# Kernel tuning notes

Measured on AMD Instinct MI355X. Metric: run time of the kernel, lower is better.

The kernel has to match this reference:

```python
import jax, jax.numpy as jnp
import numpy as np


def setup_inputs() -> dict:
    key = jax.random.key(0)
    k1, k2, k3, k4 = jax.random.split(key, 4)
    B, Lq, La, H = 8, 2048, 2048, 1024
    return {
        "q": jax.random.normal(k1, (B, Lq, H), dtype=jnp.float32),
        "a": jax.random.normal(k2, (B, La, H), dtype=jnp.float32),
        "w": jax.random.normal(k3, (H, H), dtype=jnp.float32),
        "b": jax.random.normal(k4, (H,), dtype=jnp.float32),
    }


def reference(q, a, w, b):
    # G = (q @ w + b) @ a^T : [B, Lq, La]
    G = jnp.einsum("bqh,hk->bqk", q, w) + b  # [B, Lq, H]
    G = jnp.einsum("bqh,bah->bqa", G, a)     # [B, Lq, La]
    # softmax over dim=1 (the q-length axis), no scaling
    G = jax.nn.softmax(G, axis=1)
    # H = G^T @ q : [B, La, H]
    return jnp.einsum("bqa,bqh->bah", G, q)
```

## Files before the change

kernel.cpp:

```cpp
#include <hip/hip_runtime.h>
#include <hip/hip_bf16.h>
#include <stdint.h>


typedef __bf16 bf16x8 __attribute__((ext_vector_type(8)));
typedef float f32x4 __attribute__((ext_vector_type(4)));
typedef unsigned int u32x4 __attribute__((ext_vector_type(4)));

typedef const __attribute__((address_space(1))) void* gas_t;
typedef __attribute__((address_space(3))) void* las_t;

__device__ __forceinline__ void gload_lds16(const void* g, void* l) {
    __builtin_amdgcn_global_load_lds((gas_t)g, (las_t)l, 16, 0, 0);
}

__device__ __forceinline__ unsigned cvt_pk_bf16(float a, float b) {
    unsigned r;
    asm("v_cvt_pk_bf16_f32 %0, %1, %2" : "=v"(r) : "v"(a), "v"(b));
    return r;
}

__device__ __forceinline__ void split8(f32x4 x0, f32x4 x1, bf16x8& hv, bf16x8& lv) {
    float xs[8];
#pragma unroll
    for (int i = 0; i < 4; ++i) { xs[i] = x0[i]; xs[4 + i] = x1[i]; }
    u32x4 hp, lp;
#pragma unroll
    for (int i = 0; i < 4; ++i) {
        float a = xs[2 * i], b = xs[2 * i + 1];
        unsigned p = cvt_pk_bf16(a, b);
        float ra = __uint_as_float(p << 16);
        float rb = __uint_as_float(p & 0xffff0000u);
        hp[i] = p;
        lp[i] = cvt_pk_bf16(a - ra, b - rb);
    }
    hv = __builtin_bit_cast(bf16x8, hp);
    lv = __builtin_bit_cast(bf16x8, lp);
}

#define MFMA16(a, b, c) __builtin_amdgcn_mfma_f32_16x16x32_bf16(a, b, c, 0, 0, 0)

template<bool BIAS, bool OUTSPLIT>
__global__ __launch_bounds__(256, 2) void gemm_splitAB(
    const float* __restrict__ A, const unsigned short* __restrict__ Bh,
    const unsigned short* __restrict__ Bl, const float* __restrict__ bias,
    float* __restrict__ C, unsigned short* __restrict__ Ph, unsigned short* __restrict__ Pl,
    int lda, int ldb, int ldc, int K, size_t sA, size_t sB, size_t sC)
{
    __shared__ char sm[32768];
    const int tid = threadIdx.x;
    const int lane = tid & 63, wid = tid >> 6;
    const int wr = wid >> 1, wc = wid & 1;
    const int bm = blockIdx.y * 128, bn = blockIdx.x * 128;

    const float* Ag = A + (size_t)blockIdx.z * sA;
    const unsigned short* Bhg = Bh + (size_t)blockIdx.z * sB;
    const unsigned short* Blg = Bl + (size_t)blockIdx.z * sB;

    const int a_rl = lane >> 3, a_s = lane & 7;
    const int a_kslot = a_s ^ a_rl;
    const int b_rl = lane >> 2, b_s = lane & 3;
    const int b_kslot = b_s ^ (b_rl & 3);

    const int frow = lane & 15, fkg = lane >> 4;

    f32x4 acc[4][4] = {};

    for (int k0 = 0; k0 < K; k0 += 32) {
        __syncthreads();
#pragma unroll
        for (int j = 0; j < 4; ++j) {
            int i = wid * 4 + j;
            int row = i * 8 + a_rl;
            gload_lds16(Ag + (size_t)(bm + row) * lda + (k0 + a_kslot * 4),
                        sm + i * 1024);
        }
#pragma unroll
        for (int j = 0; j < 2; ++j) {
            int i = wid * 2 + j;
            int row = i * 16 + b_rl;
            size_t goff = (size_t)(bn + row) * ldb + (k0 + b_kslot * 8);
            gload_lds16(Bhg + goff, sm + 16384 + i * 1024);
            gload_lds16(Blg + goff, sm + 24576 + i * 1024);
        }
        __syncthreads();

        bf16x8 ah[4], al[4];
#pragma unroll
        for (int m = 0; m < 4; ++m) {
            int r = wr * 64 + m * 16 + frow;
            const char* base = sm + r * 128;
            f32x4 x0 = *(const f32x4*)(base + (((2 * fkg) ^ (r & 7)) * 16));
            f32x4 x1 = *(const f32x4*)(base + (((2 * fkg + 1) ^ (r & 7)) * 16));
            split8(x0, x1, ah[m], al[m]);
        }
        bf16x8 bh[4], bl[4];
#pragma unroll
        for (int n = 0; n < 4; ++n) {
            int r = wc * 64 + n * 16 + frow;
            int off = r * 64 + ((fkg ^ (r & 3)) * 16);
            bh[n] = *(const bf16x8*)(sm + 16384 + off);
            bl[n] = *(const bf16x8*)(sm + 24576 + off);
        }
#pragma unroll
        for (int m = 0; m < 4; ++m)
#pragma unroll
            for (int n = 0; n < 4; ++n) {
                acc[m][n] = MFMA16(ah[m], bh[n], acc[m][n]);
                acc[m][n] = MFMA16(ah[m], bl[n], acc[m][n]);
                acc[m][n] = MFMA16(al[m], bh[n], acc[m][n]);
            }
    }

    const size_t zC = (size_t)blockIdx.z * sC;
    const int crow0 = bm + wr * 64 + (lane >> 4) * 4;
    const int ccol0 = bn + wc * 64 + (lane & 15);
#pragma unroll
    for (int n = 0; n < 4; ++n) {
        int col = ccol0 + n * 16;
        float bv = BIAS ? bias[col] : 0.0f;
#pragma unroll
        for (int m = 0; m < 4; ++m)
#pragma unroll
            for (int j = 0; j < 4; ++j) {
                int row = crow0 + m * 16 + j;
                float v = acc[m][n][j] + bv;
                size_t idx = zC + (size_t)row * ldc + col;
                if (OUTSPLIT) {
                    unsigned p = cvt_pk_bf16(v, v);
                    float rh = __uint_as_float(p << 16);
                    unsigned pl2 = cvt_pk_bf16(v - rh, v - rh);
                    Ph[idx] = (unsigned short)(p & 0xffffu);
                    Pl[idx] = (unsigned short)(pl2 & 0xffffu);
                } else {
                    C[idx] = v;
                }
            }
    }
}

__global__ __launch_bounds__(256, 2) void gemm_bf16(
    const unsigned short* __restrict__ A, const unsigned short* __restrict__ B,
    float* __restrict__ C, int lda, int ldb, int ldc, int K,
    size_t sA, size_t sB, size_t sC)
{
    __shared__ char sm[16384];
    const int tid = threadIdx.x;
    const int lane = tid & 63, wid = tid >> 6;
    const int wr = wid >> 1, wc = wid & 1;
    const int bm = blockIdx.y * 128, bn = blockIdx.x * 128;

    const unsigned short* Ag = A + (size_t)blockIdx.z * sA;
    const unsigned short* Bg = B + (size_t)blockIdx.z * sB;

    const int b_rl = lane >> 2, b_s = lane & 3;
    const int b_kslot = b_s ^ (b_rl & 3);
    const int frow = lane & 15, fkg = lane >> 4;

    f32x4 acc[4][4] = {};

    for (int k0 = 0; k0 < K; k0 += 32) {
        __syncthreads();
#pragma unroll
        for (int j = 0; j < 2; ++j) {
            int i = wid * 2 + j;
            int row = i * 16 + b_rl;
            gload_lds16(Ag + (size_t)(bm + row) * lda + (k0 + b_kslot * 8),
                        sm + i * 1024);
            gload_lds16(Bg + (size_t)(bn + row) * ldb + (k0 + b_kslot * 8),
                        sm + 8192 + i * 1024);
        }
        __syncthreads();

        bf16x8 af[4], bf[4];
#pragma unroll
        for (int m = 0; m < 4; ++m) {
            int r = wr * 64 + m * 16 + frow;
            af[m] = *(const bf16x8*)(sm + r * 64 + ((fkg ^ (r & 3)) * 16));
        }
#pragma unroll
        for (int n = 0; n < 4; ++n) {
            int r = wc * 64 + n * 16 + frow;
            bf[n] = *(const bf16x8*)(sm + 8192 + r * 64 + ((fkg ^ (r & 3)) * 16));
        }
#pragma unroll
        for (int m = 0; m < 4; ++m)
#pragma unroll
            for (int n = 0; n < 4; ++n)
                acc[m][n] = MFMA16(af[m], bf[n], acc[m][n]);
    }

    const size_t zC = (size_t)blockIdx.z * sC;
    const int crow0 = bm + wr * 64 + (lane >> 4) * 4;
    const int ccol0 = bn + wc * 64 + (lane & 15);
#pragma unroll
    for (int m = 0; m < 4; ++m)
#pragma unroll
        for (int n = 0; n < 4; ++n)
#pragma unroll
            for (int j = 0; j < 4; ++j)
                C[zC + (size_t)(crow0 + m * 16 + j) * ldc + ccol0 + n * 16] = acc[m][n][j];
}

__global__ void transpose_split_w(const float* __restrict__ w,
                                  unsigned short* __restrict__ th,
                                  unsigned short* __restrict__ tl)
{
    __shared__ float t[32][33];
    const int bx = blockIdx.x * 32, by = blockIdx.y * 32;
    const int tx = threadIdx.x & 31, ty = threadIdx.x >> 5;
#pragma unroll
    for (int j = 0; j < 4; ++j)
        t[ty + 8 * j][tx] = w[(size_t)(by + ty + 8 * j) * 1024 + bx + tx];
    __syncthreads();
#pragma unroll
    for (int j = 0; j < 4; ++j) {
        float v = t[tx][ty + 8 * j];
        size_t o = (size_t)(bx + ty + 8 * j) * 1024 + by + tx;
        unsigned p = cvt_pk_bf16(v, v);
        float rh = __uint_as_float(p << 16);
        unsigned p2 = cvt_pk_bf16(v - rh, v - rh);
        th[o] = (unsigned short)(p & 0xffffu);
        tl[o] = (unsigned short)(p2 & 0xffffu);
    }
}

__global__ void transpose_q_bf16(const float* __restrict__ q,
                                 unsigned short* __restrict__ qT)
{
    __shared__ float t[32][33];
    const int bx = blockIdx.x * 32, by = blockIdx.y * 32;
    const int tx = threadIdx.x & 31, ty = threadIdx.x >> 5;
    const size_t zin = (size_t)blockIdx.z * 2048 * 1024;
#pragma unroll
    for (int j = 0; j < 4; ++j)
        t[ty + 8 * j][tx] = q[zin + (size_t)(by + ty + 8 * j) * 1024 + bx + tx];
    __syncthreads();
#pragma unroll
    for (int j = 0; j < 4; ++j) {
        float v = t[tx][ty + 8 * j];
        unsigned p = cvt_pk_bf16(v, v);
        qT[zin + (size_t)(bx + ty + 8 * j) * 2048 + by + tx] = (unsigned short)(p & 0xffffu);
    }
}

__global__ __launch_bounds__(256) void softmax2048_bf16(float* __restrict__ S, size_t batchStride)
{
    float* row = S + (size_t)blockIdx.y * batchStride + (size_t)blockIdx.x * 2048;
    const int tid = threadIdx.x;
    const int lane = tid & 63, wid = tid >> 6;

    float x[8];
    *(float4*)&x[0] = *(const float4*)(row + tid * 4);
    *(float4*)&x[4] = *(const float4*)(row + 1024 + tid * 4);

    float m = x[0];
#pragma unroll
    for (int i = 1; i < 8; ++i) m = fmaxf(m, x[i]);
#pragma unroll
    for (int o = 1; o < 64; o <<= 1) m = fmaxf(m, __shfl_xor(m, o));

    __shared__ float smax[4], ssum[4];
    if (lane == 0) smax[wid] = m;
    __syncthreads();
    m = fmaxf(fmaxf(smax[0], smax[1]), fmaxf(smax[2], smax[3]));

    float e[8], s = 0.0f;
#pragma unroll
    for (int i = 0; i < 8; ++i) { e[i] = __expf(x[i] - m); s += e[i]; }
#pragma unroll
    for (int o = 1; o < 64; o <<= 1) s += __shfl_xor(s, o);
    if (lane == 0) ssum[wid] = s;
    __syncthreads();
    s = (ssum[0] + ssum[1]) + (ssum[2] + ssum[3]);

    const float inv = 1.0f / s;
    unsigned short* orow = (unsigned short*)row;
    uint2 w0, w1;
    w0.x = cvt_pk_bf16(e[0] * inv, e[1] * inv);
    w0.y = cvt_pk_bf16(e[2] * inv, e[3] * inv);
    w1.x = cvt_pk_bf16(e[4] * inv, e[5] * inv);
    w1.y = cvt_pk_bf16(e[6] * inv, e[7] * inv);
    *(uint2*)(orow + tid * 4) = w0;
    *(uint2*)(orow + 1024 + tid * 4) = w1;
}

extern "C" void kernel_launch(void* const* d_in, const int* in_sizes, int n_in,
                              void* d_out, int out_size, void* d_ws, size_t ws_size,
                              hipStream_t stream)
{
    const float* q  = (const float*)d_in[0];
    const float* a  = (const float*)d_in[1];
    const float* w  = (const float*)d_in[2];
    const float* bv = (const float*)d_in[3];
    float* out = (float*)d_out;

    const int B = 8, LQ = 2048, LA = 2048, H = 1024;
    const size_t qB = (size_t)LQ * H;

    unsigned short* wTh = (unsigned short*)d_ws;
    unsigned short* wTl = wTh + (size_t)H * H;
    unsigned short* qT  = wTl + (size_t)H * H;
    unsigned short* ph  = qT + (size_t)B * H * LQ;
    unsigned short* pl  = ph + (size_t)B * qB;
    float* S = (float*)(pl + (size_t)B * qB);

    transpose_split_w<<<dim3(32, 32), 256, 0, stream>>>(w, wTh, wTl);
    transpose_q_bf16<<<dim3(32, 64, 8), 256, 0, stream>>>(q, qT);

    gemm_splitAB<true, true><<<dim3(8, 128, 1), 256, 0, stream>>>(
        q, wTh, wTl, bv, nullptr, ph, pl, H, H, H, H, 0, 0, 0);

    for (int c = 0; c < 2; ++c) {
        const float* ac = a + (size_t)c * 4 * qB;
        const unsigned short* phc = ph + (size_t)c * 4 * qB;
        const unsigned short* plc = pl + (size_t)c * 4 * qB;
        gemm_splitAB<false, false><<<dim3(16, 16, 4), 256, 0, stream>>>(
            ac, phc, plc, nullptr, S, nullptr, nullptr,
            H, H, LQ, H, (size_t)LA * H, qB, (size_t)LA * LQ);
        softmax2048_bf16<<<dim3(LA, 4), 256, 0, stream>>>(S, (size_t)LA * LQ);
        gemm_bf16<<<dim3(8, 16, 4), 256, 0, stream>>>(
            (const unsigned short*)S, qT + (size_t)c * 4 * H * LQ,
            out + (size_t)c * 4 * LA * H,
            2 * LQ, LQ, H, LQ,
            (size_t)LA * 2 * LQ, (size_t)H * LQ, (size_t)LA * H);
    }
}
```

Before: 692.0 us.

## Rewrite split-bf16 GEMM as 256x256 double-buffered pipelined kernel

Replaces the 128x128 single-buffered three-pass split-bf16 GEMM with a 512-thread 256x256 tile kernel that double-buffers A/B tiles in 128KB of dynamic LDS. Loads for the next K-step are interleaved between MFMA groups with explicit vmcnt waits, and s_setprio raises priority around the MFMA groups. Workgroup IDs are remapped to spread blocks across XCDs. The aim is to hide global load latency and raise reuse per tile, at the cost of large LDS use (one block per CU) and fewer workgroups in the grid.

```diff
diff --git a/kernel.cpp b/kernel.cpp
--- a/kernel.cpp
+++ b/kernel.cpp
@@ -6,6 +6,7 @@
 typedef __bf16 bf16x8 __attribute__((ext_vector_type(8)));
 typedef float f32x4 __attribute__((ext_vector_type(4)));
 typedef unsigned int u32x4 __attribute__((ext_vector_type(4)));
+typedef unsigned short ushort_t;
 
 typedef const __attribute__((address_space(1))) void* gas_t;
 typedef __attribute__((address_space(3))) void* las_t;
@@ -41,86 +42,143 @@
 #define MFMA16(a, b, c) __builtin_amdgcn_mfma_f32_16x16x32_bf16(a, b, c, 0, 0, 0)
 
 template<bool BIAS, bool OUTSPLIT>
-__global__ __launch_bounds__(256, 2) void gemm_splitAB(
-    const float* __restrict__ A, const unsigned short* __restrict__ Bh,
-    const unsigned short* __restrict__ Bl, const float* __restrict__ bias,
-    float* __restrict__ C, unsigned short* __restrict__ Ph, unsigned short* __restrict__ Pl,
+__global__ __launch_bounds__(512, 2) void gemm3p(
+    const float* __restrict__ A, const ushort_t* __restrict__ Bh,
+    const ushort_t* __restrict__ Bl, const float* __restrict__ bias,
+    float* __restrict__ C, ushort_t* __restrict__ Ph, ushort_t* __restrict__ Pl,
     int lda, int ldb, int ldc, int K, size_t sA, size_t sB, size_t sC)
 {
-    __shared__ char sm[32768];
-    const int tid = threadIdx.x;
-    const int lane = tid & 63, wid = tid >> 6;
-    const int wr = wid >> 1, wc = wid & 1;
-    const int bm = blockIdx.y * 128, bn = blockIdx.x * 128;
+    extern __shared__ char sm[];
+
+    const int nwg = gridDim.x * gridDim.y;
+    int bidl = blockIdx.y * gridDim.x + blockIdx.x;
+    bidl = (bidl & 7) * (nwg >> 3) + (bidl >> 3);
+    const int bx = bidl % gridDim.x, by = bidl / gridDim.x;
+    const int bm = by * 256, bn = bx * 256;
 
     const float* Ag = A + (size_t)blockIdx.z * sA;
-    const unsigned short* Bhg = Bh + (size_t)blockIdx.z * sB;
-    const unsigned short* Blg = Bl + (size_t)blockIdx.z * sB;
-
-    const int a_rl = lane >> 3, a_s = lane & 7;
-    const int a_kslot = a_s ^ a_rl;
-    const int b_rl = lane >> 2, b_s = lane & 3;
-    const int b_kslot = b_s ^ (b_rl & 3);
-
+    const ushort_t* Bhg = Bh + (size_t)blockIdx.z * sB;
+    const ushort_t* Blg = Bl + (size_t)blockIdx.z * sB;
+
+    const int tid = threadIdx.x, lane = tid & 63, wid = tid >> 6;
+    const int wr = wid >> 2, wc = wid & 3;
     const int frow = lane & 15, fkg = lane >> 4;
 
-    f32x4 acc[4][4] = {};
-
-    for (int k0 = 0; k0 < K; k0 += 32) {
-        __syncthreads();
-#pragma unroll
-        for (int j = 0; j < 4; ++j) {
-            int i = wid * 4 + j;
-            int row = i * 8 + a_rl;
-            gload_lds16(Ag + (size_t)(bm + row) * lda + (k0 + a_kslot * 4),
-                        sm + i * 1024);
-        }
-#pragma unroll
-        for (int j = 0; j < 2; ++j) {
-            int i = wid * 2 + j;
-            int row = i * 16 + b_rl;
-            size_t goff = (size_t)(bn + row) * ldb + (k0 + b_kslot * 8);
-            gload_lds16(Bhg + goff, sm + 16384 + i * 1024);
-            gload_lds16(Blg + goff, sm + 24576 + i * 1024);
-        }
-        __syncthreads();
-
-        bf16x8 ah[4], al[4];
+    const int a_r = wid * 8 + (lane >> 3), a_s = lane & 7;
+    const int b_r = wid * 16 + (lane >> 2), b_s = lane & 3;
+    const int ldst = wid * 1024 + lane * 16;
+
+    auto stageA2 = [&](int k0, char* wb, int i0) {
+#pragma unroll
+        for (int ii = 0; ii < 2; ++ii) {
+            int i = i0 + ii;
+            int row = i * 64 + a_r;
+            gload_lds16(Ag + (size_t)(bm + row) * lda + k0 + ((a_s ^ (row & 7)) << 2),
+                        wb + i * 8192 + ldst);
+        }
+    };
+    auto stageB = [&](const ushort_t* Bg, int k0, char* dst) {
+#pragma unroll
+        for (int i = 0; i < 2; ++i) {
+            int row = i * 128 + b_r;
+            gload_lds16(Bg + (size_t)(bn + row) * ldb + k0 + ((b_s ^ (row & 3)) << 3),
+                        dst + i * 8192 + ldst);
+        }
+    };
+
+    f32x4 acc[8][4] = {};
+
+    stageA2(0, sm, 0);
+    stageA2(0, sm, 2);
+    stageB(Bhg, 0, sm + 32768);
+    stageB(Blg, 0, sm + 49152);
+    asm volatile("s_waitcnt vmcnt(2)" ::: "memory");
+    __builtin_amdgcn_s_barrier();
+
+    const int NT = K >> 5;
+    for (int t = 0; t < NT; ++t) {
+        char* rb = sm + (t & 1) * 65536;
+        char* wb = sm + ((t + 1) & 1) * 65536;
+        const int kn = ((t + 1) & (NT - 1)) << 5;
+
+        bf16x8 ah[8], al[8], bh[4], bl[4];
+
 #pragma unroll
         for (int m = 0; m < 4; ++m) {
-            int r = wr * 64 + m * 16 + frow;
-            const char* base = sm + r * 128;
+            int r = wr * 128 + m * 16 + frow;
+            const char* base = rb + r * 128;
             f32x4 x0 = *(const f32x4*)(base + (((2 * fkg) ^ (r & 7)) * 16));
             f32x4 x1 = *(const f32x4*)(base + (((2 * fkg + 1) ^ (r & 7)) * 16));
             split8(x0, x1, ah[m], al[m]);
         }
-        bf16x8 bh[4], bl[4];
 #pragma unroll
         for (int n = 0; n < 4; ++n) {
             int r = wc * 64 + n * 16 + frow;
-            int off = r * 64 + ((fkg ^ (r & 3)) * 16);
-            bh[n] = *(const bf16x8*)(sm + 16384 + off);
-            bl[n] = *(const bf16x8*)(sm + 24576 + off);
-        }
+            bh[n] = *(const bf16x8*)(rb + 32768 + r * 64 + ((fkg ^ (r & 3)) * 16));
+        }
+        stageA2(kn, wb, 0);
+        __builtin_amdgcn_s_setprio(1);
 #pragma unroll
         for (int m = 0; m < 4; ++m)
 #pragma unroll
-            for (int n = 0; n < 4; ++n) {
+            for (int n = 0; n < 4; ++n)
                 acc[m][n] = MFMA16(ah[m], bh[n], acc[m][n]);
+        __builtin_amdgcn_s_setprio(0);
+
+#pragma unroll
+        for (int m = 4; m < 8; ++m) {
+            int r = wr * 128 + m * 16 + frow;
+            const char* base = rb + r * 128;
+            f32x4 x0 = *(const f32x4*)(base + (((2 * fkg) ^ (r & 7)) * 16));
+            f32x4 x1 = *(const f32x4*)(base + (((2 * fkg + 1) ^ (r & 7)) * 16));
+            split8(x0, x1, ah[m], al[m]);
+        }
+        stageA2(kn, wb, 2);
+        __builtin_amdgcn_s_setprio(1);
+#pragma unroll
+        for (int m = 4; m < 8; ++m)
+#pragma unroll
+            for (int n = 0; n < 4; ++n)
+                acc[m][n] = MFMA16(ah[m], bh[n], acc[m][n]);
+        __builtin_amdgcn_s_setprio(0);
+        asm volatile("s_waitcnt vmcnt(4)" ::: "memory");
+        __builtin_amdgcn_s_barrier();
+
+#pragma unroll
+        for (int n = 0; n < 4; ++n) {
+            int r = wc * 64 + n * 16 + frow;
+            bl[n] = *(const bf16x8*)(rb + 49152 + r * 64 + ((fkg ^ (r & 3)) * 16));
+        }
+        stageB(Bhg, kn, wb + 32768);
+        __builtin_amdgcn_s_setprio(1);
+#pragma unroll
+        for (int m = 0; m < 8; ++m)
+#pragma unroll
+            for (int n = 0; n < 4; ++n)
                 acc[m][n] = MFMA16(ah[m], bl[n], acc[m][n]);
+        __builtin_amdgcn_s_setprio(0);
+
+        stageB(Blg, kn, wb + 49152);
+        __builtin_amdgcn_s_setprio(1);
+#pragma unroll
+        for (int m = 0; m < 8; ++m)
+#pragma unroll
+            for (int n = 0; n < 4; ++n)
                 acc[m][n] = MFMA16(al[m], bh[n], acc[m][n]);
-            }
+        __builtin_amdgcn_s_setprio(0);
+        asm volatile("s_waitcnt vmcnt(2)" ::: "memory");
+        __builtin_amdgcn_s_barrier();
     }
 
     const size_t zC = (size_t)blockIdx.z * sC;
-    const int crow0 = bm + wr * 64 + (lane >> 4) * 4;
-    const int ccol0 = bn + wc * 64 + (lane & 15);
+    const int crow0 = bm + wr * 128 + fkg * 4;
+    const int ccol0 = bn + wc * 64 + frow;
 #pragma unroll
     for (int n = 0; n < 4; ++n) {
         int col = ccol0 + n * 16;
         float bv = BIAS ? bias[col] : 0.0f;
 #pragma unroll
-        for (int m = 0; m < 4; ++m)
+        for (int m = 0; m < 8; ++m)
 #pragma unroll
             for (int j = 0; j < 4; ++j) {
                 int row = crow0 + m * 16 + j;
@@ -130,8 +188,8 @@
                     unsigned p = cvt_pk_bf16(v, v);
                     float rh = __uint_as_float(p << 16);
                     unsigned pl2 = cvt_pk_bf16(v - rh, v - rh);
-                    Ph[idx] = (unsigned short)(p & 0xffffu);
-                    Pl[idx] = (unsigned short)(pl2 & 0xffffu);
+                    Ph[idx] = (ushort_t)(p & 0xffffu);
+                    Pl[idx] = (ushort_t)(pl2 & 0xffffu);
                 } else {
                     C[idx] = v;
                 }
@@ -140,7 +198,7 @@
 }
 
 __global__ __launch_bounds__(256, 2) void gemm_bf16(
-    const unsigned short* __restrict__ A, const unsigned short* __restrict__ B,
+    const ushort_t* __restrict__ A, const ushort_t* __restrict__ B,
     float* __restrict__ C, int lda, int ldb, int ldc, int K,
     size_t sA, size_t sB, size_t sC)
 {
@@ -150,8 +208,8 @@
     const int wr = wid >> 1, wc = wid & 1;
     const int bm = blockIdx.y * 128, bn = blockIdx.x * 128;
 
-    const unsigned short* Ag = A + (size_t)blockIdx.z * sA;
-    const unsigned short* Bg = B + (size_t)blockIdx.z * sB;
+    const ushort_t* Ag = A + (size_t)blockIdx.z * sA;
+    const ushort_t* Bg = B + (size_t)blockIdx.z * sB;
 
     const int b_rl = lane >> 2, b_s = lane & 3;
     const int b_kslot = b_s ^ (b_rl & 3);
@@ -203,8 +261,8 @@
 }
 
 __global__ void transpose_split_w(const float* __restrict__ w,
-                                  unsigned short* __restrict__ th,
-                                  unsigned short* __restrict__ tl)
+                                  ushort_t* __restrict__ th,
+                                  ushort_t* __restrict__ tl)
 {
     __shared__ float t[32][33];
     const int bx = blockIdx.x * 32, by = blockIdx.y * 32;
@@ -220,13 +278,13 @@
         unsigned p = cvt_pk_bf16(v, v);
         float rh = __uint_as_float(p << 16);
         unsigned p2 = cvt_pk_bf16(v - rh, v - rh);
-        th[o] = (unsigned short)(p & 0xffffu);
-        tl[o] = (unsigned short)(p2 & 0xffffu);
+        th[o] = (ushort_t)(p & 0xffffu);
+        tl[o] = (ushort_t)(p2 & 0xffffu);
     }
 }
 
 __global__ void transpose_q_bf16(const float* __restrict__ q,
-                                 unsigned short* __restrict__ qT)
+                                 ushort_t* __restrict__ qT)
 {
     __shared__ float t[32][33];
     const int bx = blockIdx.x * 32, by = blockIdx.y * 32;
@@ -240,7 +298,7 @@
     for (int j = 0; j < 4; ++j) {
         float v = t[tx][ty + 8 * j];
         unsigned p = cvt_pk_bf16(v, v);
-        qT[zin + (size_t)(bx + ty + 8 * j) * 2048 + by + tx] = (unsigned short)(p & 0xffffu);
+        qT[zin + (size_t)(bx + ty + 8 * j) * 2048 + by + tx] = (ushort_t)(p & 0xffffu);
     }
 }
 
@@ -275,7 +333,7 @@
     s = (ssum[0] + ssum[1]) + (ssum[2] + ssum[3]);
 
     const float inv = 1.0f / s;
-    unsigned short* orow = (unsigned short*)row;
+    ushort_t* orow = (ushort_t*)row;
     uint2 w0, w1;
     w0.x = cvt_pk_bf16(e[0] * inv, e[1] * inv);
     w0.y = cvt_pk_bf16(e[2] * inv, e[3] * inv);
@@ -298,29 +356,29 @@
     const int B = 8, LQ = 2048, LA = 2048, H = 1024;
     const size_t qB = (size_t)LQ * H;
 
-    unsigned short* wTh = (unsigned short*)d_ws;
-    unsigned short* wTl = wTh + (size_t)H * H;
-    unsigned short* qT  = wTl + (size_t)H * H;
-    unsigned short* ph  = qT + (size_t)B * H * LQ;
-    unsigned short* pl  = ph + (size_t)B * qB;
+    ushort_t* wTh = (ushort_t*)d_ws;
+    ushort_t* wTl = wTh + (size_t)H * H;
+    ushort_t* qT  = wTl + (size_t)H * H;
+    ushort_t* ph  = qT + (size_t)B * H * LQ;
+    ushort_t* pl  = ph + (size_t)B * qB;
     float* S = (float*)(pl + (size_t)B * qB);
 
     transpose_split_w<<<dim3(32, 32), 256, 0, stream>>>(w, wTh, wTl);
     transpose_q_bf16<<<dim3(32, 64, 8), 256, 0, stream>>>(q, qT);
 
-    gemm_splitAB<true, true><<<dim3(8, 128, 1), 256, 0, stream>>>(
+    gemm3p<true, true><<<dim3(4, 64, 1), 512, 131072, stream>>>(
         q, wTh, wTl, bv, nullptr, ph, pl, H, H, H, H, 0, 0, 0);
 
     for (int c = 0; c < 2; ++c) {
         const float* ac = a + (size_t)c * 4 * qB;
-        const unsigned short* phc = ph + (size_t)c * 4 * qB;
-        const unsigned short* plc = pl + (size_t)c * 4 * qB;
-        gemm_splitAB<false, false><<<dim3(16, 16, 4), 256, 0, stream>>>(
+        const ushort_t* phc = ph + (size_t)c * 4 * qB;
+        const ushort_t* plc = pl + (size_t)c * 4 * qB;
+        gemm3p<false, false><<<dim3(8, 8, 4), 512, 131072, stream>>>(
             ac, phc, plc, nullptr, S, nullptr, nullptr,
             H, H, LQ, H, (size_t)LA * H, qB, (size_t)LA * LQ);
         softmax2048_bf16<<<dim3(LA, 4), 256, 0, stream>>>(S, (size_t)LA * LQ);
         gemm_bf16<<<dim3(8, 16, 4), 256, 0, stream>>>(
-            (const unsigned short*)S, qT + (size_t)c * 4 * H * LQ,
+            (const ushort_t*)S, qT + (size_t)c * 4 * H * LQ,
             out + (size_t)c * 4 * LA * H,
             2 * LQ, LQ, H, LQ,
             (size_t)LA * 2 * LQ, (size_t)H * LQ, (size_t)LA * H);
```

Result: faster. 623.5 us (-9.9%).
